# Kernel optimization log

Measured on AMD Instinct MI355X. Metric: run time of the kernel, lower is better.

Reference implementation:

```python
import jax, jax.numpy as jnp
import numpy as np

B, T, S, H, V, L = 2048, 48, 128, 256, 96, 2


def setup_inputs() -> dict:
    key = jax.random.key(0)
    ks = jax.random.split(key, 16)
    s = 0.05
    y = jax.random.randint(ks[0], (B, T), 0, V)
    encoder_outputs = jax.random.normal(ks[1], (B, S, H), jnp.float32)
    encoder_hidden = jax.random.normal(ks[2], (L, B, H), jnp.float32)
    params = {
        'W_ih0': jax.random.normal(ks[3], (3 * H, V + H), jnp.float32) * s,
        'W_hh0': jax.random.normal(ks[4], (3 * H, H), jnp.float32) * s,
        'b_ih0': jax.random.normal(ks[5], (3 * H,), jnp.float32) * s,
        'b_hh0': jax.random.normal(ks[6], (3 * H,), jnp.float32) * s,
        'W_ih1': jax.random.normal(ks[7], (3 * H, H), jnp.float32) * s,
        'W_hh1': jax.random.normal(ks[8], (3 * H, H), jnp.float32) * s,
        'b_ih1': jax.random.normal(ks[9], (3 * H,), jnp.float32) * s,
        'b_hh1': jax.random.normal(ks[10], (3 * H,), jnp.float32) * s,
        'wc_W': jax.random.normal(ks[11], (H, 2 * H), jnp.float32) * s,
        'wc_b': jax.random.normal(ks[12], (H,), jnp.float32) * s,
        'ws_W': jax.random.normal(ks[13], (V, H), jnp.float32) * s,
        'ws_b': jax.random.normal(ks[14], (V,), jnp.float32) * s,
    }
    return dict(y=y, encoder_outputs=encoder_outputs, encoder_hidden=encoder_hidden,
                is_training=1, **params)


def _gru_cell(x, h, Wih, Whh, bih, bhh):
    # PyTorch GRUCell math
    gi = x @ Wih.T + bih
    gh = h @ Whh.T + bhh
    ir, iz, inn = jnp.split(gi, 3, axis=-1)
    hr, hz, hn = jnp.split(gh, 3, axis=-1)
    r = jax.nn.sigmoid(ir + hr)
    z = jax.nn.sigmoid(iz + hz)
    n = jnp.tanh(inn + r * hn)
    return (1.0 - z) * n + z * h


def reference(y, encoder_outputs, encoder_hidden, is_training,
              W_ih0, W_hh0, b_ih0, b_hh0, W_ih1, W_hh1, b_ih1, b_hh1,
              wc_W, wc_b, ws_W, ws_b):
    # Teacher-forcing (is_training=True) path; embedding is fixed one-hot.
    vocab = ws_W.shape[0]
    xs = jax.nn.one_hot(y[:, :-1], vocab, dtype=encoder_outputs.dtype)  # [B,T-1,V]
    xs = jnp.swapaxes(xs, 0, 1)  # [T-1,B,V]
    h0, h1 = encoder_hidden[0], encoder_hidden[1]
    last_ht = jnp.zeros_like(h0)

    def step(carry, x_t):
        lht, c0, c1 = carry
        rnn_in = jnp.concatenate([x_t, lht], axis=-1)  # [B, V+H]
        c0n = _gru_cell(rnn_in, c0, W_ih0, W_hh0, b_ih0, b_hh0)
        c1n = _gru_cell(c0n, c1, W_ih1, W_hh1, b_ih1, b_hh1)
        out = c1n  # GRU top-layer output, [B,H]
        energy = jnp.einsum('bsh,bh->bs', encoder_outputs, out)
        alpha = jax.nn.softmax(energy, axis=-1)
        ctx = jnp.einsum('bs,bsh->bh', alpha, encoder_outputs)
        ht = jnp.tanh(jnp.concatenate([out, ctx], axis=-1) @ wc_W.T + wc_b)
        logits = ht @ ws_W.T + ws_b  # [B,V]
        return (ht, c0n, c1n), logits

    _, outs = jax.lax.scan(step, (last_ht, h0, h1), xs)
    return jnp.swapaxes(outs, 0, 1)  # [B, T-1, V]
```

## Files before the change

### kernel.cpp

```cpp
#include <hip/hip_runtime.h>

#define BATCH 2048
#define TTOT 48
#define TOUT 47
#define SS 128
#define HH 256
#define VV 96
#define MB 8
#define NBLK (BATCH / MB)
#define NTHR 1024

#define OFF_T0I 0
#define OFF_T0H 196608
#define OFF_T1I 393216
#define OFF_T1H 589824
#define OFF_TG  786432
#define OFF_TC  860160
#define OFF_TS  991232
#define WS_FLOATS 1015808

struct __align__(16) SMem {
    float ht[MB * 256];
    float c0[MB * 256];
    float c1[MB * 256];
    float cx[MB * 256];
    float g[12 * 2048];
    float Dp[2][MB];
    float Mp[2][MB];
    int   ym[MB];
};

__device__ __forceinline__ float dot4(const float4 a, const float4 b) {
    return a.x * b.x + a.y * b.y + a.z * b.z + a.w * b.w;
}

__device__ __forceinline__ float wave_sum64(float v) {
    v += __int_as_float(__builtin_amdgcn_update_dpp(0, __float_as_int(v), 0x111, 0xf, 0xf, true));
    v += __int_as_float(__builtin_amdgcn_update_dpp(0, __float_as_int(v), 0x112, 0xf, 0xf, true));
    v += __int_as_float(__builtin_amdgcn_update_dpp(0, __float_as_int(v), 0x114, 0xf, 0xf, true));
    v += __int_as_float(__builtin_amdgcn_update_dpp(0, __float_as_int(v), 0x118, 0xf, 0xf, true));
    v += __int_as_float(__builtin_amdgcn_update_dpp(0, __float_as_int(v), 0x142, 0xa, 0xf, true));
    v += __int_as_float(__builtin_amdgcn_update_dpp(0, __float_as_int(v), 0x143, 0xc, 0xf, true));
    return __int_as_float(__builtin_amdgcn_readlane(__float_as_int(v), 63));
}

__device__ __forceinline__ void gru_gemv(
    const float* __restrict__ TI, const float* __restrict__ TH,
    const float* __restrict__ bih, const float* __restrict__ bhh,
    const float* xS, const float* hS, float* g, const int tid)
{
    const int kh = tid >> 9;
    const int side = (tid >> 8) & 1;
    const int i0 = tid & 255;
    const float* __restrict__ bW = (side ? TH : TI) + (size_t)kh * 98304;
    const float* __restrict__ bias = side ? bhh : bih;
    const float* sk = (side ? hS : xS) + kh * 128;
    float a0[MB], a1[MB], a2[MB];
    const float b0v = kh ? 0.f : bias[i0];
    const float b1v = kh ? 0.f : bias[i0 + 256];
    const float b2v = kh ? 0.f : bias[i0 + 512];
    #pragma unroll
    for (int m = 0; m < MB; ++m) { a0[m] = b0v; a1[m] = b1v; a2[m] = b2v; }
    #pragma unroll 2
    for (int kk = 0; kk < 32; ++kk) {
        const float4 w0 = *(const float4*)(bW + ((size_t)kk * 768 + i0) * 4);
        const float4 w1 = *(const float4*)(bW + ((size_t)kk * 768 + i0 + 256) * 4);
        const float4 w2 = *(const float4*)(bW + ((size_t)kk * 768 + i0 + 512) * 4);
        #pragma unroll
        for (int m = 0; m < MB; ++m) {
            const float4 s4 = *(const float4*)(sk + m * 256 + kk * 4);
            a0[m] += dot4(w0, s4);
            a1[m] += dot4(w1, s4);
            a2[m] += dot4(w2, s4);
        }
    }
    const int cb = (kh * 2 + side) * 3 * 2048;
    #pragma unroll
    for (int m = 0; m < MB; ++m) {
        g[cb + m * 256 + i0]            = a0[m];
        g[cb + 2048 + m * 256 + i0]     = a1[m];
        g[cb + 4096 + m * 256 + i0]     = a2[m];
    }
}

template <bool GATHER>
__device__ __forceinline__ void gru_update(
    const float* g, float* st, const float* __restrict__ TG, const int* ym, const int tid)
{
    for (int p = tid; p < MB * 256; p += NTHR) {
        const int m = p >> 8, c = p & 255;
        const float* gm = g + m * 256 + c;
        float iR = gm[0 * 2048] + gm[6 * 2048];
        float hR = gm[3 * 2048] + gm[9 * 2048];
        float iZ = gm[1 * 2048] + gm[7 * 2048];
        float hZ = gm[4 * 2048] + gm[10 * 2048];
        float iN = gm[2 * 2048] + gm[8 * 2048];
        const float hN = gm[5 * 2048] + gm[11 * 2048];
        if (GATHER) {
            const float* tg = TG + (size_t)ym[m] * 768;
            iR += tg[c]; iZ += tg[256 + c]; iN += tg[512 + c];
        }
        const float r = 1.f / (1.f + __expf(-(iR + hR)));
        const float z = 1.f / (1.f + __expf(-(iZ + hZ)));
        const float n = tanhf(iN + r * hN);
        st[p] = (1.f - z) * n + z * st[p];
    }
}

__global__ __launch_bounds__(NTHR, 4) void decoder_kernel(
    const int* __restrict__ y,
    const float* __restrict__ enc,
    const float* __restrict__ eh,
    const float* __restrict__ bih0,
    const float* __restrict__ bhh0,
    const float* __restrict__ bih1,
    const float* __restrict__ bhh1,
    const float* __restrict__ wcb,
    const float* __restrict__ wsb,
    const float* __restrict__ ws,
    float* __restrict__ out)
{
    __shared__ SMem sm;
    const int tid = threadIdx.x;
    const int b0 = blockIdx.x * MB;

    const float* __restrict__ T0I = ws + OFF_T0I;
    const float* __restrict__ T0H = ws + OFF_T0H;
    const float* __restrict__ T1I = ws + OFF_T1I;
    const float* __restrict__ T1H = ws + OFF_T1H;
    const float* __restrict__ TG  = ws + OFF_TG;
    const float* __restrict__ TC  = ws + OFF_TC;
    const float* __restrict__ TS  = ws + OFF_TS;

    for (int idx = tid; idx < MB * 256; idx += NTHR) {
        sm.ht[idx] = 0.f;
        sm.c0[idx] = eh[b0 * HH + idx];
        sm.c1[idx] = eh[(size_t)BATCH * HH + b0 * HH + idx];
    }
    __syncthreads();

    for (int t = 0; t < TOUT; ++t) {
        if (tid < MB) sm.ym[tid] = y[(b0 + tid) * TTOT + t];

        gru_gemv(T0I, T0H, bih0, bhh0, sm.ht, sm.c0, sm.g, tid);
        __syncthreads();
        gru_update<true>(sm.g, sm.c0, TG, sm.ym, tid);
        __syncthreads();

        gru_gemv(T1I, T1H, bih1, bhh1, sm.c0, sm.c1, sm.g, tid);
        __syncthreads();
        gru_update<false>(sm.g, sm.c1, TG, sm.ym, tid);
        __syncthreads();

        {
            const int m = tid >> 7, sh = (tid >> 6) & 1, lane = tid & 63;
            const float4 o4 = *(const float4*)(sm.c1 + m * 256 + lane * 4);
            const float* er = enc + ((size_t)(b0 + m) * SS + sh * 64) * HH + lane * 4;
            float4 C = {0.f, 0.f, 0.f, 0.f};
            float D = 0.f, Mx = -3.0e38f;
            for (int s = 0; s < 64; s += 2) {
                const float4 a4 = *(const float4*)(er);
                const float4 b4 = *(const float4*)(er + HH);
                er += 2 * HH;
                const float e0 = wave_sum64(dot4(a4, o4));
                const float e1 = wave_sum64(dot4(b4, o4));
                const float nm = fmaxf(Mx, fmaxf(e0, e1));
                const float sc = __expf(Mx - nm);
                const float p0 = __expf(e0 - nm);
                const float p1 = __expf(e1 - nm);
                D = D * sc + p0 + p1;
                C.x = C.x * sc + p0 * a4.x + p1 * b4.x;
                C.y = C.y * sc + p0 * a4.y + p1 * b4.y;
                C.z = C.z * sc + p0 * a4.z + p1 * b4.z;
                C.w = C.w * sc + p0 * a4.w + p1 * b4.w;
                Mx = nm;
            }
            *(float4*)(sm.g + (sh * 8 + m) * 256 + lane * 4) = C;
            if (lane == 0) { sm.Dp[sh][m] = D; sm.Mp[sh][m] = Mx; }
        }
        __syncthreads();
        for (int p = tid; p < MB * 256; p += NTHR) {
            const int m = p >> 8, h = p & 255;
            const float M0 = sm.Mp[0][m], M1 = sm.Mp[1][m];
            const float Mt = fmaxf(M0, M1);
            const float e0 = __expf(M0 - Mt), e1 = __expf(M1 - Mt);
            const float den = sm.Dp[0][m] * e0 + sm.Dp[1][m] * e1;
            const float num = sm.g[m * 256 + h] * e0 + sm.g[(8 + m) * 256 + h] * e1;
            sm.cx[p] = num / den;
        }
        __syncthreads();

        {
            const int i0w = tid & 127;
            const int sel = (tid >> 7) & 1;
            const int khf = (tid >> 8) & 1;
            const int mh  = tid >> 9;
            const float* st = (sel ? sm.cx : sm.c1) + khf * 128;
            const float* base = TC + ((size_t)sel * 16384 + (size_t)khf * 8192) * 4;
            float a0[4], a1[4];
            #pragma unroll
            for (int q = 0; q < 4; ++q) { a0[q] = 0.f; a1[q] = 0.f; }
            #pragma unroll 2
            for (int kk = 0; kk < 32; ++kk) {
                const float4 w0 = *(const float4*)(base + ((size_t)kk * 256 + i0w) * 4);
                const float4 w1 = *(const float4*)(base + ((size_t)kk * 256 + i0w + 128) * 4);
                #pragma unroll
                for (int q = 0; q < 4; ++q) {
                    const float4 s4 = *(const float4*)(st + (mh * 4 + q) * 256 + kk * 4);
                    a0[q] += dot4(w0, s4);
                    a1[q] += dot4(w1, s4);
                }
            }
            #pragma unroll
            for (int q = 0; q < 4; ++q) {
                const int m = mh * 4 + q;
                sm.g[((sel * 2 + khf) * 8 + m) * 256 + i0w]       = a0[q];
                sm.g[((sel * 2 + khf) * 8 + m) * 256 + i0w + 128] = a1[q];
            }
        }
        __syncthreads();
        for (int p = tid; p < MB * 256; p += NTHR) {
            const int m = p >> 8, i = p & 255;
            sm.ht[p] = tanhf(sm.g[(0 * 8 + m) * 256 + i] + sm.g[(1 * 8 + m) * 256 + i]
                           + sm.g[(2 * 8 + m) * 256 + i] + sm.g[(3 * 8 + m) * 256 + i]
                           + wcb[i]);
        }
        __syncthreads();

        for (int p = tid; p < MB * VV; p += NTHR) {
            const int m = p / VV, v = p - m * VV;
            const float* h = sm.ht + m * 256;
            float acc = wsb[v];
            #pragma unroll 4
            for (int k4 = 0; k4 < 64; ++k4)
                acc += dot4(*(const float4*)(TS + ((size_t)k4 * 96 + v) * 4),
                            *(const float4*)(h + k4 * 4));
            out[(size_t)((b0 + m) * TOUT + t) * VV + v] = acc;
        }
    }
}

__global__ __launch_bounds__(256) void prep_kernel(
    const float* __restrict__ Wih0, const float* __restrict__ Whh0,
    const float* __restrict__ Wih1, const float* __restrict__ Whh1,
    const float* __restrict__ wcW,  const float* __restrict__ wsW,
    float* __restrict__ ws)
{
    const int idx = blockIdx.x * 256 + threadIdx.x;
    if (idx < OFF_T0H) {
        const int j = idx & 3, q = idx >> 2;
        const int i = q % 768, k4 = q / 768;
        ws[idx] = Wih0[i * 352 + 96 + k4 * 4 + j];
    } else if (idx < OFF_T1I) {
        const int v = idx - OFF_T0H;
        const int j = v & 3, q = v >> 2;
        const int i = q % 768, k4 = q / 768;
        ws[idx] = Whh0[i * 256 + k4 * 4 + j];
    } else if (idx < OFF_T1H) {
        const int v = idx - OFF_T1I;
        const int j = v & 3, q = v >> 2;
        const int i = q % 768, k4 = q / 768;
        ws[idx] = Wih1[i * 256 + k4 * 4 + j];
    } else if (idx < OFF_TG) {
        const int v = idx - OFF_T1H;
        const int j = v & 3, q = v >> 2;
        const int i = q % 768, k4 = q / 768;
        ws[idx] = Whh1[i * 256 + k4 * 4 + j];
    } else if (idx < OFF_TC) {
        const int v = idx - OFF_TG;
        const int col = v / 768, i = v % 768;
        ws[idx] = Wih0[i * 352 + col];
    } else if (idx < OFF_TS) {
        const int v = idx - OFF_TC;
        const int j = v & 3, q = v >> 2;
        const int i = q & 255, q2 = q >> 8;
        const int k4 = q2 & 63, sel = q2 >> 6;
        ws[idx] = wcW[i * 512 + sel * 256 + k4 * 4 + j];
    } else if (idx < WS_FLOATS) {
        const int v = idx - OFF_TS;
        const int j = v & 3, q = v >> 2;
        const int vv = q % 96, k4 = q / 96;
        ws[idx] = wsW[vv * 256 + k4 * 4 + j];
    }
}

extern "C" void kernel_launch(void* const* d_in, const int* in_sizes, int n_in,
                              void* d_out, int out_size, void* d_ws, size_t ws_size,
                              hipStream_t stream) {
    (void)in_sizes; (void)n_in; (void)out_size; (void)ws_size;
    const int* y = (const int*)d_in[0];
    const float* enc  = (const float*)d_in[1];
    const float* eh   = (const float*)d_in[2];
    const float* Wih0 = (const float*)d_in[4];
    const float* Whh0 = (const float*)d_in[5];
    const float* bih0 = (const float*)d_in[6];
    const float* bhh0 = (const float*)d_in[7];
    const float* Wih1 = (const float*)d_in[8];
    const float* Whh1 = (const float*)d_in[9];
    const float* bih1 = (const float*)d_in[10];
    const float* bhh1 = (const float*)d_in[11];
    const float* wcW  = (const float*)d_in[12];
    const float* wcb  = (const float*)d_in[13];
    const float* wsW  = (const float*)d_in[14];
    const float* wsb  = (const float*)d_in[15];
    float* outp = (float*)d_out;
    float* wsp  = (float*)d_ws;

    prep_kernel<<<dim3(WS_FLOATS / 256), dim3(256), 0, stream>>>(
        Wih0, Whh0, Wih1, Whh1, wcW, wsW, wsp);
    decoder_kernel<<<dim3(NBLK), dim3(NTHR), 0, stream>>>(
        y, enc, eh, bih0, bhh0, bih1, bhh1, wcb, wsb, wsp, outp);
}
```

Baseline: 6.804 ms.

## Use split-fp16 MFMA for GRU and combine GEMVs instead of fp32 dot products

Replaces the fp32 FMA GEMVs for both GRU layers and the attention-combine layer with 16x16x32 fp16 MFMA instructions. Weights and activations are each split into a hi and lo fp16 pair to keep near-fp32 accuracy, and the two K-halves are reduced with a DPP row rotate. The prep kernel now writes weights in MFMA fragment order, and biases are added in the elementwise update step. This aims to cut ALU-bound matvec time, at the cost of extra passes, fp16 conversions on every state update and more complex indexing.

```diff
diff --git a/kernel.cpp b/kernel.cpp
--- a/kernel.cpp
+++ b/kernel.cpp
@@ -1,4 +1,5 @@
 #include <hip/hip_runtime.h>
+#include <hip/hip_fp16.h>
 
 #define BATCH 2048
 #define TTOT 48
@@ -10,21 +11,36 @@
 #define NBLK (BATCH / MB)
 #define NTHR 1024
 
-#define OFF_T0I 0
-#define OFF_T0H 196608
-#define OFF_T1I 393216
-#define OFF_T1H 589824
-#define OFF_TG  786432
-#define OFF_TC  860160
-#define OFF_TS  991232
-#define WS_FLOATS 1015808
+#define F0I_OFF 0
+#define F0H_OFF 393216
+#define F1I_OFF 786432
+#define F1H_OFF 1179648
+#define FC_OFF  1572864
+#define FRAG_USHORTS 1835008
+#define TG_OFF 917504
+#define TS_OFF 991232
+
+typedef __attribute__((ext_vector_type(8))) _Float16 half8v;
+typedef __attribute__((ext_vector_type(4))) float f32x4;
+
+__device__ __forceinline__ unsigned short f2h(float f) {
+    const __half h = __float2half_rn(f);
+    return *reinterpret_cast<const unsigned short*>(&h);
+}
+__device__ __forceinline__ float h2f(unsigned short u) {
+    const __half h = *reinterpret_cast<const __half*>(&u);
+    return __half2float(h);
+}
 
 struct __align__(16) SMem {
     float ht[MB * 256];
     float c0[MB * 256];
     float c1[MB * 256];
-    float cx[MB * 256];
-    float g[12 * 2048];
+    float gT[2][MB][776];
+    unsigned short htB[2][MB][264];
+    unsigned short c0B[2][MB][264];
+    unsigned short c1B[2][MB][264];
+    unsigned short cxB[2][MB][264];
     float Dp[2][MB];
     float Mp[2][MB];
     int   ym[MB];
@@ -32,6 +48,10 @@
 
 __device__ __forceinline__ float dot4(const float4 a, const float4 b) {
     return a.x * b.x + a.y * b.y + a.z * b.z + a.w * b.w;
+}
+
+__device__ __forceinline__ float ror8f(float v) {
+    return __int_as_float(__builtin_amdgcn_update_dpp(0, __float_as_int(v), 0x128, 0xf, 0xf, true));
 }
 
 __device__ __forceinline__ float wave_sum64(float v) {
@@ -44,66 +64,41 @@
     return __int_as_float(__builtin_amdgcn_readlane(__float_as_int(v), 63));
 }
 
-__device__ __forceinline__ void gru_gemv(
-    const float* __restrict__ TI, const float* __restrict__ TH,
-    const float* __restrict__ bih, const float* __restrict__ bhh,
-    const float* xS, const float* hS, float* g, const int tid)
+__device__ __forceinline__ void gru_mfma(
+    const unsigned short* __restrict__ F,
+    const unsigned short* xB, const unsigned short* hB,
+    float* gT, const int tid)
 {
-    const int kh = tid >> 9;
-    const int side = (tid >> 8) & 1;
-    const int i0 = tid & 255;
-    const float* __restrict__ bW = (side ? TH : TI) + (size_t)kh * 98304;
-    const float* __restrict__ bias = side ? bhh : bih;
-    const float* sk = (side ? hS : xS) + kh * 128;
-    float a0[MB], a1[MB], a2[MB];
-    const float b0v = kh ? 0.f : bias[i0];
-    const float b1v = kh ? 0.f : bias[i0 + 256];
-    const float b2v = kh ? 0.f : bias[i0 + 512];
+    const int w = tid >> 6, lane = tid & 63;
+    const int side = w >> 3, wq = w & 7;
+    const unsigned short* bst = side ? hB : xB;
+    const unsigned short* bp = bst + ((lane >> 3) & 1) * 2112 + (lane & 7) * 264 + ((lane >> 4) << 3);
+    half8v Bf[8];
     #pragma unroll
-    for (int m = 0; m < MB; ++m) { a0[m] = b0v; a1[m] = b1v; a2[m] = b2v; }
-    #pragma unroll 2
-    for (int kk = 0; kk < 32; ++kk) {
-        const float4 w0 = *(const float4*)(bW + ((size_t)kk * 768 + i0) * 4);
-        const float4 w1 = *(const float4*)(bW + ((size_t)kk * 768 + i0 + 256) * 4);
-        const float4 w2 = *(const float4*)(bW + ((size_t)kk * 768 + i0 + 512) * 4);
+    for (int k = 0; k < 8; ++k) Bf[k] = *(const half8v*)(bp + k * 32);
+    const unsigned short* Fw = F + (size_t)side * 393216 + wq * 512 + lane * 8;
+    f32x4 acc[6];
+    #pragma unroll
+    for (int r = 0; r < 6; ++r) acc[r] = (f32x4){0.f, 0.f, 0.f, 0.f};
+    #pragma unroll
+    for (int pk = 0; pk < 16; ++pk) {
+        const unsigned short* fa = Fw + (size_t)pk * (48 * 512);
         #pragma unroll
-        for (int m = 0; m < MB; ++m) {
-            const float4 s4 = *(const float4*)(sk + m * 256 + kk * 4);
-            a0[m] += dot4(w0, s4);
-            a1[m] += dot4(w1, s4);
-            a2[m] += dot4(w2, s4);
-        }
-    }
-    const int cb = (kh * 2 + side) * 3 * 2048;
+        for (int r = 0; r < 6; ++r) {
+            const half8v A = *(const half8v*)(fa + r * (8 * 512));
+            acc[r] = __builtin_amdgcn_mfma_f32_16x16x32_f16(A, Bf[pk & 7], acc[r], 0, 0, 0);
+        }
+    }
+    const int colm = lane & 15;
+    float* gbase = gT + (size_t)side * 6208 + (lane & 7) * 776 + ((lane >> 4) << 2);
     #pragma unroll
-    for (int m = 0; m < MB; ++m) {
-        g[cb + m * 256 + i0]            = a0[m];
-        g[cb + 2048 + m * 256 + i0]     = a1[m];
-        g[cb + 4096 + m * 256 + i0]     = a2[m];
-    }
-}
-
-template <bool GATHER>
-__device__ __forceinline__ void gru_update(
-    const float* g, float* st, const float* __restrict__ TG, const int* ym, const int tid)
-{
-    for (int p = tid; p < MB * 256; p += NTHR) {
-        const int m = p >> 8, c = p & 255;
-        const float* gm = g + m * 256 + c;
-        float iR = gm[0 * 2048] + gm[6 * 2048];
-        float hR = gm[3 * 2048] + gm[9 * 2048];
-        float iZ = gm[1 * 2048] + gm[7 * 2048];
-        float hZ = gm[4 * 2048] + gm[10 * 2048];
-        float iN = gm[2 * 2048] + gm[8 * 2048];
-        const float hN = gm[5 * 2048] + gm[11 * 2048];
-        if (GATHER) {
-            const float* tg = TG + (size_t)ym[m] * 768;
-            iR += tg[c]; iZ += tg[256 + c]; iN += tg[512 + c];
-        }
-        const float r = 1.f / (1.f + __expf(-(iR + hR)));
-        const float z = 1.f / (1.f + __expf(-(iZ + hZ)));
-        const float n = tanhf(iN + r * hN);
-        st[p] = (1.f - z) * n + z * st[p];
+    for (int r = 0; r < 6; ++r) {
+        f32x4 s;
+        s.x = acc[r].x + ror8f(acc[r].x);
+        s.y = acc[r].y + ror8f(acc[r].y);
+        s.z = acc[r].z + ror8f(acc[r].z);
+        s.w = acc[r].w + ror8f(acc[r].w);
+        if (colm < 8) *(f32x4*)(gbase + (wq + r * 8) * 16) = s;
     }
 }
 
@@ -117,39 +112,72 @@
     const float* __restrict__ bhh1,
     const float* __restrict__ wcb,
     const float* __restrict__ wsb,
-    const float* __restrict__ ws,
+    const unsigned short* __restrict__ wsU,
     float* __restrict__ out)
 {
     __shared__ SMem sm;
     const int tid = threadIdx.x;
     const int b0 = blockIdx.x * MB;
-
-    const float* __restrict__ T0I = ws + OFF_T0I;
-    const float* __restrict__ T0H = ws + OFF_T0H;
-    const float* __restrict__ T1I = ws + OFF_T1I;
-    const float* __restrict__ T1H = ws + OFF_T1H;
-    const float* __restrict__ TG  = ws + OFF_TG;
-    const float* __restrict__ TC  = ws + OFF_TC;
-    const float* __restrict__ TS  = ws + OFF_TS;
-
-    for (int idx = tid; idx < MB * 256; idx += NTHR) {
-        sm.ht[idx] = 0.f;
-        sm.c0[idx] = eh[b0 * HH + idx];
-        sm.c1[idx] = eh[(size_t)BATCH * HH + b0 * HH + idx];
+    const float* __restrict__ wsF = (const float*)wsU;
+    const float* __restrict__ TG = wsF + TG_OFF;
+    const float* __restrict__ TS = wsF + TS_OFF;
+
+    for (int p = tid; p < MB * 256; p += NTHR) {
+        const int m = p >> 8, c = p & 255;
+        sm.ht[p] = 0.f;
+        sm.htB[0][m][c] = 0; sm.htB[1][m][c] = 0;
+        const float v0 = eh[b0 * HH + p];
+        const float v1 = eh[(size_t)BATCH * HH + b0 * HH + p];
+        sm.c0[p] = v0; sm.c1[p] = v1;
+        const unsigned short h0 = f2h(v0);
+        sm.c0B[0][m][c] = h0; sm.c0B[1][m][c] = f2h(v0 - h2f(h0));
+        const unsigned short h1 = f2h(v1);
+        sm.c1B[0][m][c] = h1; sm.c1B[1][m][c] = f2h(v1 - h2f(h1));
     }
     __syncthreads();
 
     for (int t = 0; t < TOUT; ++t) {
         if (tid < MB) sm.ym[tid] = y[(b0 + tid) * TTOT + t];
 
-        gru_gemv(T0I, T0H, bih0, bhh0, sm.ht, sm.c0, sm.g, tid);
-        __syncthreads();
-        gru_update<true>(sm.g, sm.c0, TG, sm.ym, tid);
-        __syncthreads();
-
-        gru_gemv(T1I, T1H, bih1, bhh1, sm.c0, sm.c1, sm.g, tid);
-        __syncthreads();
-        gru_update<false>(sm.g, sm.c1, TG, sm.ym, tid);
+        gru_mfma(wsU + F0I_OFF, &sm.htB[0][0][0], &sm.c0B[0][0][0], &sm.gT[0][0][0], tid);
+        __syncthreads();
+        for (int p = tid; p < MB * 256; p += NTHR) {
+            const int m = p >> 8, c = p & 255;
+            const float* tg = TG + (size_t)sm.ym[m] * 768;
+            const float iR = sm.gT[0][m][c]       + bih0[c]       + tg[c];
+            const float hR = sm.gT[1][m][c]       + bhh0[c];
+            const float iZ = sm.gT[0][m][256 + c] + bih0[256 + c] + tg[256 + c];
+            const float hZ = sm.gT[1][m][256 + c] + bhh0[256 + c];
+            const float iN = sm.gT[0][m][512 + c] + bih0[512 + c] + tg[512 + c];
+            const float hN = sm.gT[1][m][512 + c] + bhh0[512 + c];
+            const float r = 1.f / (1.f + __expf(-(iR + hR)));
+            const float z = 1.f / (1.f + __expf(-(iZ + hZ)));
+            const float n = tanhf(iN + r * hN);
+            const float v = (1.f - z) * n + z * sm.c0[p];
+            sm.c0[p] = v;
+            const unsigned short hb = f2h(v);
+            sm.c0B[0][m][c] = hb; sm.c0B[1][m][c] = f2h(v - h2f(hb));
+        }
+        __syncthreads();
+
+        gru_mfma(wsU + F1I_OFF, &sm.c0B[0][0][0], &sm.c1B[0][0][0], &sm.gT[0][0][0], tid);
+        __syncthreads();
+        for (int p = tid; p < MB * 256; p += NTHR) {
+            const int m = p >> 8, c = p & 255;
+            const float iR = sm.gT[0][m][c]       + bih1[c];
+            const float hR = sm.gT[1][m][c]       + bhh1[c];
+            const float iZ = sm.gT[0][m][256 + c] + bih1[256 + c];
+            const float hZ = sm.gT[1][m][256 + c] + bhh1[256 + c];
+            const float iN = sm.gT[0][m][512 + c] + bih1[512 + c];
+            const float hN = sm.gT[1][m][512 + c] + bhh1[512 + c];
+            const float r = 1.f / (1.f + __expf(-(iR + hR)));
+            const float z = 1.f / (1.f + __expf(-(iZ + hZ)));
+            const float n = tanhf(iN + r * hN);
+            const float v = (1.f - z) * n + z * sm.c1[p];
+            sm.c1[p] = v;
+            const unsigned short hb = f2h(v);
+            sm.c1B[0][m][c] = hb; sm.c1B[1][m][c] = f2h(v - h2f(hb));
+        }
         __syncthreads();
 
         {
@@ -175,7 +203,7 @@
                 C.w = C.w * sc + p0 * a4.w + p1 * b4.w;
                 Mx = nm;
             }
-            *(float4*)(sm.g + (sh * 8 + m) * 256 + lane * 4) = C;
+            *(float4*)(&sm.gT[sh][m][lane * 4]) = C;
             if (lane == 0) { sm.Dp[sh][m] = D; sm.Mp[sh][m] = Mx; }
         }
         __syncthreads();
@@ -185,45 +213,41 @@
             const float Mt = fmaxf(M0, M1);
             const float e0 = __expf(M0 - Mt), e1 = __expf(M1 - Mt);
             const float den = sm.Dp[0][m] * e0 + sm.Dp[1][m] * e1;
-            const float num = sm.g[m * 256 + h] * e0 + sm.g[(8 + m) * 256 + h] * e1;
-            sm.cx[p] = num / den;
+            const float v = (sm.gT[0][m][h] * e0 + sm.gT[1][m][h] * e1) / den;
+            const unsigned short hb = f2h(v);
+            sm.cxB[0][m][h] = hb; sm.cxB[1][m][h] = f2h(v - h2f(hb));
         }
         __syncthreads();
 
         {
-            const int i0w = tid & 127;
-            const int sel = (tid >> 7) & 1;
-            const int khf = (tid >> 8) & 1;
-            const int mh  = tid >> 9;
-            const float* st = (sel ? sm.cx : sm.c1) + khf * 128;
-            const float* base = TC + ((size_t)sel * 16384 + (size_t)khf * 8192) * 4;
-            float a0[4], a1[4];
+            const int w = tid >> 6, lane = tid & 63;
+            const unsigned short* b1 = &sm.c1B[0][0][0] + ((lane >> 3) & 1) * 2112 + (lane & 7) * 264 + ((lane >> 4) << 3);
+            const unsigned short* b2 = &sm.cxB[0][0][0] + ((lane >> 3) & 1) * 2112 + (lane & 7) * 264 + ((lane >> 4) << 3);
+            const unsigned short* FCw = wsU + FC_OFF + w * 512 + lane * 8;
+            f32x4 acc = (f32x4){0.f, 0.f, 0.f, 0.f};
             #pragma unroll
-            for (int q = 0; q < 4; ++q) { a0[q] = 0.f; a1[q] = 0.f; }
-            #pragma unroll 2
-            for (int kk = 0; kk < 32; ++kk) {
-                const float4 w0 = *(const float4*)(base + ((size_t)kk * 256 + i0w) * 4);
-                const float4 w1 = *(const float4*)(base + ((size_t)kk * 256 + i0w + 128) * 4);
-                #pragma unroll
-                for (int q = 0; q < 4; ++q) {
-                    const float4 s4 = *(const float4*)(st + (mh * 4 + q) * 256 + kk * 4);
-                    a0[q] += dot4(w0, s4);
-                    a1[q] += dot4(w1, s4);
-                }
+            for (int pk = 0; pk < 32; ++pk) {
+                const int k = pk & 15;
+                const unsigned short* bpk = (k < 8) ? (b1 + k * 32) : (b2 + (k - 8) * 32);
+                const half8v B = *(const half8v*)bpk;
+                const half8v A = *(const half8v*)(FCw + (size_t)pk * (16 * 512));
+                acc = __builtin_amdgcn_mfma_f32_16x16x32_f16(A, B, acc, 0, 0, 0);
             }
-            #pragma unroll
-            for (int q = 0; q < 4; ++q) {
-                const int m = mh * 4 + q;
-                sm.g[((sel * 2 + khf) * 8 + m) * 256 + i0w]       = a0[q];
-                sm.g[((sel * 2 + khf) * 8 + m) * 256 + i0w + 128] = a1[q];
-            }
+            f32x4 s;
+            s.x = acc.x + ror8f(acc.x);
+            s.y = acc.y + ror8f(acc.y);
+            s.z = acc.z + ror8f(acc.z);
+            s.w = acc.w + ror8f(acc.w);
+            if ((lane & 15) < 8)
+                *(f32x4*)(&sm.gT[0][lane & 7][w * 16 + ((lane >> 4) << 2)]) = s;
         }
         __syncthreads();
         for (int p = tid; p < MB * 256; p += NTHR) {
             const int m = p >> 8, i = p & 255;
-            sm.ht[p] = tanhf(sm.g[(0 * 8 + m) * 256 + i] + sm.g[(1 * 8 + m) * 256 + i]
-                           + sm.g[(2 * 8 + m) * 256 + i] + sm.g[(3 * 8 + m) * 256 + i]
-                           + wcb[i]);
+            const float v = tanhf(sm.gT[0][m][i] + wcb[i]);
+            sm.ht[p] = v;
+            const unsigned short hb = f2h(v);
+            sm.htB[0][m][i] = hb; sm.htB[1][m][i] = f2h(v - h2f(hb));
         }
         __syncthreads();
 
@@ -244,43 +268,41 @@
     const float* __restrict__ Wih0, const float* __restrict__ Whh0,
     const float* __restrict__ Wih1, const float* __restrict__ Whh1,
     const float* __restrict__ wcW,  const float* __restrict__ wsW,
-    float* __restrict__ ws)
+    unsigned short* __restrict__ wsU)
 {
     const int idx = blockIdx.x * 256 + threadIdx.x;
-    if (idx < OFF_T0H) {
-        const int j = idx & 3, q = idx >> 2;
-        const int i = q % 768, k4 = q / 768;
-        ws[idx] = Wih0[i * 352 + 96 + k4 * 4 + j];
-    } else if (idx < OFF_T1I) {
-        const int v = idx - OFF_T0H;
-        const int j = v & 3, q = v >> 2;
-        const int i = q % 768, k4 = q / 768;
-        ws[idx] = Whh0[i * 256 + k4 * 4 + j];
-    } else if (idx < OFF_T1H) {
-        const int v = idx - OFF_T1I;
-        const int j = v & 3, q = v >> 2;
-        const int i = q % 768, k4 = q / 768;
-        ws[idx] = Wih1[i * 256 + k4 * 4 + j];
-    } else if (idx < OFF_TG) {
-        const int v = idx - OFF_T1H;
-        const int j = v & 3, q = v >> 2;
-        const int i = q % 768, k4 = q / 768;
-        ws[idx] = Whh1[i * 256 + k4 * 4 + j];
-    } else if (idx < OFF_TC) {
-        const int v = idx - OFF_TG;
-        const int col = v / 768, i = v % 768;
-        ws[idx] = Wih0[i * 352 + col];
-    } else if (idx < OFF_TS) {
-        const int v = idx - OFF_TC;
-        const int j = v & 3, q = v >> 2;
-        const int i = q & 255, q2 = q >> 8;
-        const int k4 = q2 & 63, sel = q2 >> 6;
-        ws[idx] = wcW[i * 512 + sel * 256 + k4 * 4 + j];
-    } else if (idx < WS_FLOATS) {
-        const int v = idx - OFF_TS;
-        const int j = v & 3, q = v >> 2;
-        const int vv = q % 96, k4 = q / 96;
-        ws[idx] = wsW[vv * 256 + k4 * 4 + j];
+    if (idx < FRAG_USHORTS) {
+        const float* src; int stride, koff, nT; int u = idx;
+        if (u < F0H_OFF)      { src = Wih0; stride = 352; koff = 96; nT = 48; }
+        else if (u < F1I_OFF) { src = Whh0; stride = 256; koff = 0;  nT = 48; u -= F0H_OFF; }
+        else if (u < F1H_OFF) { src = Wih1; stride = 256; koff = 0;  nT = 48; u -= F1I_OFF; }
+        else if (u < FC_OFF)  { src = Whh1; stride = 256; koff = 0;  nT = 48; u -= F1H_OFF; }
+        else                  { src = wcW;  stride = 512; koff = 0;  nT = 16; u -= FC_OFF; }
+        const int j = u & 7, l = (u >> 3) & 63;
+        const int t2 = u >> 9;
+        const int tau = t2 % nT;
+        const int pk = t2 / nT;
+        const int nK = (nT == 48) ? 8 : 16;
+        const int kap = pk % nK, pass = pk / nK;
+        const int i = tau * 16 + (l & 15);
+        const int k = kap * 32 + ((l >> 4) << 3) + j;
+        const float wv = src[(size_t)i * stride + koff + k];
+        const unsigned short hb = f2h(wv);
+        wsU[idx] = (pass == 0) ? hb : f2h(wv - h2f(hb));
+    } else {
+        const int f = idx - FRAG_USHORTS;
+        float* wsF = (float*)wsU;
+        float val;
+        if (f < 73728) {
+            const int col = f / 768, i = f % 768;
+            val = Wih0[i * 352 + col];
+        } else {
+            const int v2 = f - 73728;
+            const int j = v2 & 3, q = v2 >> 2;
+            const int vv = q % 96, k4 = q / 96;
+            val = wsW[vv * 256 + k4 * 4 + j];
+        }
+        wsF[TG_OFF + f] = val;
     }
 }
 
@@ -304,10 +326,10 @@
     const float* wsW  = (const float*)d_in[14];
     const float* wsb  = (const float*)d_in[15];
     float* outp = (float*)d_out;
-    float* wsp  = (float*)d_ws;
-
-    prep_kernel<<<dim3(WS_FLOATS / 256), dim3(256), 0, stream>>>(
-        Wih0, Whh0, Wih1, Whh1, wcW, wsW, wsp);
+    unsigned short* wsU = (unsigned short*)d_ws;
+
+    prep_kernel<<<dim3((FRAG_USHORTS + 98304) / 256), dim3(256), 0, stream>>>(
+        Wih0, Whh0, Wih1, Whh1, wcW, wsW, wsU);
     decoder_kernel<<<dim3(NBLK), dim3(NTHR), 0, stream>>>(
-        y, enc, eh, bih0, bhh0, bih1, bhh1, wcb, wsb, wsp, outp);
-}
+        y, enc, eh, bih0, bhh0, bih1, bhh1, wcb, wsb, wsU, outp);
+}
```

New measurement: 11.98 ms. 76.1% more time.
